# Kernel tuning notes

Measured on AMD Instinct MI355X. Metric: run time of the kernel, lower is better.

Reference implementation:

```python
import jax, jax.numpy as jnp
import numpy as np
import math

N_NODES = 50000
N_EDGES = 800000
IN_DIM = 128
HID = 128
OUT_DIM = 2048
N_LABEL_EDGES = 4096
POOL_RATIO = 0.5
NUM_HEADS = 8


def seg_sum(x, idx, n):
    return jax.ops.segment_sum(x, idx, num_segments=n)


def graph_conv(x, W, b, src, dst, emask, n):
    # DGL GraphConv, norm='both': D_out^-1/2 A D_in^-1/2 (x W) + b (masked edges)
    deg_out = seg_sum(emask, src, n)
    deg_in = seg_sum(emask, dst, n)
    ns = jax.lax.rsqrt(jnp.maximum(deg_out, 1.0))
    nd = jax.lax.rsqrt(jnp.maximum(deg_in, 1.0))
    h = x @ W
    msg = (h * ns[:, None])[src] * emask[:, None]
    agg = seg_sum(msg, dst, n)
    return agg * nd[:, None] + b


def conv_pool_block(x, src, dst, emask, cW, cb, sW, sb):
    # GraphConv -> ReLU -> SAGPool(top-k by GraphConv score, tanh gate) -> avg||max readout
    n = x.shape[0]
    h = jax.nn.relu(graph_conv(x, cW, cb, src, dst, emask, n))
    score = graph_conv(h, sW, sb, src, dst, emask, n)[:, 0]
    k = int(math.ceil(POOL_RATIO * n))  # static
    _, perm = jax.lax.top_k(score, k)
    h_new = h[perm] * jnp.tanh(score[perm])[:, None]
    # remap edges to the pooled node set; drop edges touching removed nodes via mask
    newid = jnp.full((n,), -1, jnp.int32).at[perm].set(jnp.arange(k, dtype=jnp.int32))
    nsrc = newid[src]
    ndst = newid[dst]
    new_mask = emask * (nsrc >= 0).astype(emask.dtype) * (ndst >= 0).astype(emask.dtype)
    nsrc = jnp.maximum(nsrc, 0)
    ndst = jnp.maximum(ndst, 0)
    readout = jnp.concatenate([h_new.mean(0), h_new.max(0)])[None, :]  # [1, 2*HID]
    return h_new, nsrc, ndst, new_mask, readout


def gat_conv(x, fcW, al, ar, lsrc, ldst, n, slope=0.2):
    # GATConv(1 -> 1, num_heads=8): head feature dim is 1
    h = x @ fcW                      # [n, heads]
    el = h * al
    er = h * ar
    e = jax.nn.leaky_relu(el[lsrc] + er[ldst], slope)  # [E_l, heads]
    emax = jax.ops.segment_max(e, ldst, num_segments=n)
    emax = jnp.where(jnp.isfinite(emax), emax, 0.0)
    ex = jnp.exp(e - emax[ldst])
    denom = seg_sum(ex, ldst, n)
    alpha = ex / jnp.maximum(denom[ldst], 1e-9)
    out = seg_sum(alpha * h[lsrc], ldst, n)            # [n, heads]
    return out[:, :, None]                             # [n, heads, 1]


def setup_inputs() -> dict:
    key = jax.random.key(0)
    ks = jax.random.split(key, 32)

    def rn(k, shape, s=0.05):
        return jax.random.normal(k, shape, jnp.float32) * s

    inp = {}
    inp['feat'] = jax.random.normal(ks[0], (N_NODES, IN_DIM), jnp.float32)
    inp['sequence_feature'] = jax.random.normal(ks[1], (1, 1024), jnp.float32)
    inp['src'] = jax.random.randint(ks[2], (N_EDGES,), 0, N_NODES, jnp.int32)
    inp['dst'] = jax.random.randint(ks[3], (N_EDGES,), 0, N_NODES, jnp.int32)
    inp['label_src'] = jax.random.randint(ks[4], (N_LABEL_EDGES,), 0, OUT_DIM, jnp.int32)
    inp['label_dst'] = jax.random.randint(ks[5], (N_LABEL_EDGES,), 0, OUT_DIM, jnp.int32)
    i = 6
    for b in range(3):
        din = IN_DIM if b == 0 else HID
        inp['cW%d' % b] = rn(ks[i], (din, HID)); i += 1
        inp['cb%d' % b] = jnp.zeros((HID,), jnp.float32)
        inp['sW%d' % b] = rn(ks[i], (HID, 1)); i += 1
        inp['sb%d' % b] = jnp.zeros((1,), jnp.float32)
    inp['lin1W'] = rn(ks[i], (2 * HID + 1024, 2 * HID)); i += 1
    inp['lin1b'] = jnp.zeros((2 * HID,), jnp.float32)
    inp['lin2W'] = rn(ks[i], (2 * HID, HID)); i += 1
    inp['lin2b'] = jnp.zeros((HID,), jnp.float32)
    inp['lin3W'] = rn(ks[i], (HID, OUT_DIM)); i += 1
    inp['lin3b'] = jnp.zeros((OUT_DIM,), jnp.float32)
    inp['gat_fcW'] = rn(ks[i], (1, NUM_HEADS)); i += 1
    inp['gat_al'] = rn(ks[i], (NUM_HEADS,)); i += 1
    inp['gat_ar'] = rn(ks[i], (NUM_HEADS,)); i += 1
    return inp


def reference(feat, sequence_feature, src, dst, label_src, label_dst,
              cW0, cb0, sW0, sb0, cW1, cb1, sW1, sb1, cW2, cb2, sW2, sb2,
              lin1W, lin1b, lin2W, lin2b, lin3W, lin3b,
              gat_fcW, gat_al, gat_ar):
    x, s, d = feat, src, dst
    emask = jnp.ones((src.shape[0],), jnp.float32)
    final = None
    for cW, cb, sW, sb in ((cW0, cb0, sW0, sb0), (cW1, cb1, sW1, sb1), (cW2, cb2, sW2, sb2)):
        x, s, d, emask, ro = conv_pool_block(x, s, d, emask, cW, cb, sW, sb)
        final = ro if final is None else final + ro
    final = jnp.concatenate([final, sequence_feature], axis=-1)  # [1, 2*HID+1024]
    f = jax.nn.relu(final @ lin1W + lin1b)
    # dropout: eval mode -> identity
    f = jax.nn.relu(f @ lin2W + lin2b)
    f = f @ lin3W + lin3b          # [1, OUT_DIM]
    ft = f.T                       # [OUT_DIM, 1]
    gat_out = gat_conv(ft, gat_fcW, gat_al, gat_ar, label_src, label_dst, OUT_DIM)
    max_value = jnp.max(gat_out, axis=1)      # [OUT_DIM, 1]
    _ = ft - jax.nn.relu(max_value)           # computed then discarded, as in source
    return ft.T
```

## Files before the change

### kernel.cpp

```cpp
#include <hip/hip_runtime.h>
#include <hip/hip_bf16.h>
#include <cmath>

#define N0 50000
#define NEDGE 800000
#define NEG_HUGE -3.402823466e38f
#define BMAX 64
#define STRIDE 128

typedef int i32x4 __attribute__((ext_vector_type(4)));
typedef __attribute__((ext_vector_type(8))) short short8v;
typedef __attribute__((ext_vector_type(4))) float f32x4;

__device__ inline float b2f(unsigned short u) { return __uint_as_float(((unsigned)u) << 16); }

__device__ inline unsigned short f2b(float f) {
    __hip_bfloat16 h = __float2bfloat16(f);
    return *(unsigned short*)&h;
}

__device__ inline unsigned fkey(float f) {
    unsigned b = __float_as_uint(f);
    if (b == 0x80000000u) b = 0u;
    return (b & 0x80000000u) ? ~b : (b | 0x80000000u);
}

__device__ inline void atomicMaxF(float* a, float v) {
    if (v >= 0.f) atomicMax((int*)a, __float_as_int(v));
    else          atomicMin((unsigned int*)a, __float_as_uint(v));
}

__global__ void k_init(float* finalv, float* f1raw, int* deg_out, int* fill,
                       int* binsA, int* binsB, float* maxbuf, int* ctrl) {
    int i = blockIdx.x * blockDim.x + threadIdx.x;
    if (i < 256) { finalv[i] = 0.f; f1raw[i] = 0.f; }
    if (i < 384) maxbuf[i] = NEG_HUGE;
    if (i < N0) { deg_out[i] = 0; fill[i] = 0; }
    if (i < 65536) { binsA[i] = 0; binsB[i] = 0; }
    if (i < 2) ctrl[8 + i] = 0;
}

__global__ __launch_bounds__(256) void k_build(
        const int* __restrict__ esrc, const int* __restrict__ edst,
        int* deg_out, int* fill, int* csr_src) {
    int t = blockIdx.x * 256 + threadIdx.x;
    int e0 = t * 4;
    if (e0 >= NEDGE) return;
    i32x4 a = __builtin_nontemporal_load((const i32x4*)(esrc + e0));
    i32x4 bq = __builtin_nontemporal_load((const i32x4*)(edst + e0));
    int s[4] = {a.x, a.y, a.z, a.w};
    int d[4] = {bq.x, bq.y, bq.z, bq.w};
#pragma unroll
    for (int kq = 0; kq < 4; ++kq) {
        atomicAdd(&deg_out[s[kq]], 1);
        int pos = atomicAdd(&fill[d[kq]], 1);
        if (pos < STRIDE) csr_src[(size_t)d[kq] * STRIDE + pos] = s[kq];
    }
}

__global__ __launch_bounds__(256) void k_rmbuild(
        const int* __restrict__ esrc, const int* __restrict__ edst,
        const int2* __restrict__ ein, int use_pair,
        const int* __restrict__ ctrl, int slot,
        const int* __restrict__ newid,
        int2* __restrict__ eout, int* __restrict__ outcnt,
        int* deg_out, int* fill, int* csr_src) {
    __shared__ int wbase[4];
    __shared__ int blkbase;
    int E = (slot < 0) ? NEDGE : ctrl[slot];
    if (blockIdx.x * 256 >= E) return;
    int i = blockIdx.x * 256 + threadIdx.x;
    int lane = threadIdx.x & 63, w = threadIdx.x >> 6;
    int ns = -1, nd = -1;
    if (i < E) {
        int s, d;
        if (use_pair) { int2 pr = ein[i]; s = pr.x; d = pr.y; }
        else { s = esrc[i]; d = edst[i]; }
        ns = newid[s]; nd = newid[d];
    }
    bool keep = (ns >= 0) && (nd >= 0);
    unsigned long long m = __ballot(keep);
    int rank = __popcll(m & ((1ull << lane) - 1ull));
    if (lane == 0) wbase[w] = __popcll(m);
    __syncthreads();
    if (threadIdx.x == 0)
        blkbase = atomicAdd(outcnt, wbase[0] + wbase[1] + wbase[2] + wbase[3]);
    __syncthreads();
    int base = blkbase;
    for (int q = 0; q < w; ++q) base += wbase[q];
    if (keep) {
        eout[base + rank] = make_int2(ns, nd);
        atomicAdd(&deg_out[ns], 1);
        int pos = atomicAdd(&fill[nd], 1);
        if (pos < STRIDE) csr_src[(size_t)nd * STRIDE + pos] = ns;
    }
}

__global__ __launch_bounds__(256) void k_gemm(
        const float* __restrict__ feat, const float* __restrict__ xprev,
        const int* __restrict__ oldid, const float* __restrict__ garr,
        const int* __restrict__ deg_out,
        const float* __restrict__ W, unsigned short* __restrict__ hpre,
        int n, int nprev, int mode) {
    __shared__ short Wt[128][136];
    __shared__ short Xt[64][136];
    __shared__ int ridx_s[64];
    __shared__ float esc_s[64];
    int tid = threadIdx.x;
    int r0 = blockIdx.x * 64;
    if (tid < 64) {
        int gr = r0 + tid;
        int ridx = 0; float esc = 0.f;
        if (gr < n) {
            if (mode == 0) {
                ridx = gr;
                esc = rsqrtf(fmaxf((float)deg_out[gr], 1.f));
            } else {
                int orow = oldid[gr];
                if ((unsigned)orow < (unsigned)nprev) {
                    ridx = orow;
                    esc = rsqrtf(fmaxf((float)deg_out[gr], 1.f)) * garr[gr];
                }
            }
        }
        ridx_s[tid] = ridx;
        esc_s[tid] = esc;
    }
    __syncthreads();
    {
        int col = tid & 127;
        int kh = tid >> 7;
#pragma unroll
        for (int c8 = 0; c8 < 8; ++c8) {
            int kb = kh * 64 + c8 * 8;
            unsigned short v[8];
#pragma unroll
            for (int j = 0; j < 8; ++j)
                v[j] = f2b(W[(size_t)(kb + j) * 128 + col]);
            *(uint4*)&Wt[col][kb] = *(uint4*)v;
        }
    }
    {
        const float* xsrc = (mode == 0) ? feat : xprev;
        int rr = tid >> 2;
        int kx = (tid & 3) * 32;
        const float4* xp = (const float4*)(xsrc + (size_t)ridx_s[rr] * 128 + kx);
#pragma unroll
        for (int c4 = 0; c4 < 8; ++c4) {
            float4 v = xp[c4];
            unsigned short u[4];
            u[0] = f2b(v.x); u[1] = f2b(v.y); u[2] = f2b(v.z); u[3] = f2b(v.w);
            *(uint2*)&Xt[rr][kx + c4 * 4] = *(uint2*)u;
        }
    }
    __syncthreads();

    int lane = tid & 63, w = tid >> 6;
    int row16 = lane & 15;
    int ko = (lane >> 4) * 8;
    f32x4 acc[8];
#pragma unroll
    for (int t = 0; t < 8; ++t) acc[t] = (f32x4){0.f, 0.f, 0.f, 0.f};
#pragma unroll
    for (int kc = 0; kc < 4; ++kc) {
        int kbase = kc * 32 + ko;
        short8v a = *(short8v*)&Xt[w * 16 + row16][kbase];
#pragma unroll
        for (int t = 0; t < 8; ++t) {
            short8v b = *(short8v*)&Wt[t * 16 + row16][kbase];
            acc[t] = __builtin_amdgcn_mfma_f32_16x16x32_bf16(a, b, acc[t], 0, 0, 0);
        }
    }
    int rq = (lane >> 4) * 4;
    float esc[4];
#pragma unroll
    for (int r = 0; r < 4; ++r) esc[r] = esc_s[w * 16 + rq + r];
#pragma unroll
    for (int r = 0; r < 4; ++r) {
        int gr = r0 + w * 16 + rq + r;
        if (gr < n) {
            unsigned short* op = hpre + (size_t)gr * 128;
#pragma unroll
            for (int t = 0; t < 8; ++t)
                op[t * 16 + (lane & 15)] = f2b(acc[t][r] * esc[r]);
        }
    }
}

__global__ __launch_bounds__(256) void k_agg_conv(
        const unsigned short* __restrict__ hpre, const int* __restrict__ fill,
        const int* __restrict__ deg_out,
        const int* __restrict__ csr_src,
        const float* __restrict__ cb, const float* __restrict__ sW,
        float* __restrict__ hpost, float* __restrict__ hs, int n) {
    int wid = threadIdx.x >> 6;
    int lane = threadIdx.x & 63;
    int d = blockIdx.x * 4 + wid;
    if (d >= n) return;
    int degin = fill[d];
    int cnt = min(degin, STRIDE);
    const int* bp = csr_src + (size_t)d * STRIDE;
    float a0 = 0.f, a1 = 0.f;
    int j = 0;
    for (; j + 4 <= cnt; j += 4) {
        int4 ss = *(const int4*)(bp + j);
        ushort2 u0 = ((const ushort2*)(hpre + (size_t)ss.x * 128))[lane];
        ushort2 u1 = ((const ushort2*)(hpre + (size_t)ss.y * 128))[lane];
        ushort2 u2 = ((const ushort2*)(hpre + (size_t)ss.z * 128))[lane];
        ushort2 u3 = ((const ushort2*)(hpre + (size_t)ss.w * 128))[lane];
        a0 += (b2f(u0.x) + b2f(u1.x)) + (b2f(u2.x) + b2f(u3.x));
        a1 += (b2f(u0.y) + b2f(u1.y)) + (b2f(u2.y) + b2f(u3.y));
    }
    for (; j < cnt; ++j) {
        int s0 = bp[j];
        ushort2 u0 = ((const ushort2*)(hpre + (size_t)s0 * 128))[lane];
        a0 += b2f(u0.x);
        a1 += b2f(u0.y);
    }
    float nd2 = rsqrtf(fmaxf((float)degin, 1.f));
    int c0 = lane * 2;
    float h0 = fmaxf(fmaf(a0, nd2, cb[c0]), 0.f);
    float h1 = fmaxf(fmaf(a1, nd2, cb[c0 + 1]), 0.f);
    ((float2*)(hpost + (size_t)d * 128))[lane] = make_float2(h0, h1);
    float v = h0 * sW[c0] + h1 * sW[c0 + 1];
#pragma unroll
    for (int off = 32; off; off >>= 1) v += __shfl_down(v, off);
    if (lane == 0) hs[d] = v * rsqrtf(fmaxf((float)deg_out[d], 1.f));
}

__global__ void k_score_hist(const float* __restrict__ hs, const int* __restrict__ fill,
                             const int* __restrict__ csr_src,
                             const float* __restrict__ sb, float* score,
                             int* binsA, int n) {
    int d = blockIdx.x * blockDim.x + threadIdx.x;
    if (d >= n) return;
    int degin = fill[d];
    int cnt = min(degin, STRIDE);
    const int* bp = csr_src + (size_t)d * STRIDE;
    float sum = 0.f;
    int j = 0;
    for (; j + 4 <= cnt; j += 4) {
        int4 ss = *(const int4*)(bp + j);
        sum += (hs[ss.x] + hs[ss.y]) + (hs[ss.z] + hs[ss.w]);
    }
    for (; j < cnt; ++j) sum += hs[bp[j]];
    float sc = rsqrtf(fmaxf((float)degin, 1.f)) * sum + sb[0];
    score[d] = sc;
    atomicAdd(&binsA[fkey(sc) >> 16], 1);
}

__global__ void k_rhist2(const float* __restrict__ score, const int* __restrict__ ctrl,
                         int n, int* binsB) {
    unsigned p16 = (unsigned)ctrl[3];
    for (int i = blockIdx.x * 256 + threadIdx.x; i < n; i += gridDim.x * 256) {
        unsigned u = fkey(score[i]);
        if ((u >> 16) == p16) atomicAdd(&binsB[u & 0xFFFFu], 1);
    }
}

__global__ void k_rpick(int stage, int k0, int* ctrl, const int* __restrict__ bins) {
    __shared__ int gs[64];
    __shared__ int arr[1024];
    __shared__ int wsum[16];
    __shared__ int sChunk, sKrem;
    int t = threadIdx.x;
    {
        int c = t >> 4, sub = t & 15;
        const int4* p4 = (const int4*)(bins + (size_t)c * 1024);
        int s = 0;
#pragma unroll
        for (int q = 0; q < 16; ++q) {
            int4 v = p4[q * 16 + sub];
            s += v.x + v.y + v.z + v.w;
        }
#pragma unroll
        for (int off = 8; off; off >>= 1) s += __shfl_down(s, off, 16);
        if (sub == 0) gs[c] = s;
    }
    __syncthreads();
    if (t == 0) {
        int kneed = (stage == 0) ? k0 : ctrl[4];
        int cum = 0, c = 63;
        for (; c >= 1; --c) { int v = gs[c]; if (cum + v >= kneed) break; cum += v; }
        sChunk = c; sKrem = kneed - cum;
    }
    __syncthreads();
    int c = sChunk;
    int v = bins[(size_t)c * 1024 + t];
    arr[t] = v;
    int lane = t & 63, w = t >> 6;
    int s = v;
#pragma unroll
    for (int off = 32; off; off >>= 1) s += __shfl_down(s, off);
    if (lane == 0) wsum[w] = s;
    __syncthreads();
    if (t == 0) {
        int kneed = sKrem;
        int cum = 0, w2 = 15;
        for (; w2 >= 1; --w2) { int vv = wsum[w2]; if (cum + vv >= kneed) break; cum += vv; }
        int j = 63;
        for (; j >= 1; --j) { int vv = arr[w2 * 64 + j]; if (cum + vv >= kneed) break; cum += vv; }
        int bin = c * 1024 + w2 * 64 + j;
        if (stage == 0) { ctrl[3] = bin; ctrl[4] = kneed - cum; }
        else {
            ctrl[0] = (int)((((unsigned)ctrl[3]) << 16) | (unsigned)bin);
            ctrl[2] = kneed - cum;
        }
    }
}

__global__ void k_ccnt(const float* __restrict__ score, const int* __restrict__ ctrl,
                       int n, int* cntG, int* cntE) {
    __shared__ int wG[16], wE[16];
    int b = blockIdx.x;
    int i = b * 1024 + threadIdx.x;
    int lane = threadIdx.x & 63, wid = threadIdx.x >> 6;
    unsigned T = (unsigned)ctrl[0];
    bool inb = (i < n);
    unsigned u = inb ? fkey(score[i]) : 0u;
    bool isG = inb && (u > T);
    bool isE = inb && (u == T);
    unsigned long long mG = __ballot(isG);
    unsigned long long mE = __ballot(isE);
    if (lane == 0) { wG[wid] = __popcll(mG); wE[wid] = __popcll(mE); }
    __syncthreads();
    if (threadIdx.x == 0) {
        int sg = 0, se = 0;
#pragma unroll
        for (int w = 0; w < 16; ++w) { sg += wG[w]; se += wE[w]; }
        cntG[b] = sg; cntE[b] = se;
    }
}

__global__ void k_cemit(const float* __restrict__ score, const int* __restrict__ ctrl,
                        const int* __restrict__ cntG, const int* __restrict__ cntE,
                        int n, int knext, int* newid, int* oldid, float* garr,
                        int* deg_out, int* fill, int* binsA, int* binsB) {
    __shared__ int wG[16], wE[16];
    __shared__ int sGoff, sEoff;
    int b = blockIdx.x;
    int i = b * 1024 + threadIdx.x;
    if (knext > 0) {
        for (int z = i; z < 65536; z += gridDim.x * 1024) { binsA[z] = 0; binsB[z] = 0; }
        if (i < knext) { deg_out[i] = 0; fill[i] = 0; }
    }
    int lane = threadIdx.x & 63, wid = threadIdx.x >> 6;
    unsigned T = (unsigned)ctrl[0];
    int needEq = ctrl[2];
    bool inb = (i < n);
    float sc = inb ? score[i] : 0.f;
    unsigned u = inb ? fkey(sc) : 0u;
    bool isG = inb && (u > T);
    bool isE = inb && (u == T);
    unsigned long long mG = __ballot(isG);
    unsigned long long mE = __ballot(isE);
    if (lane == 0) { wG[wid] = __popcll(mG); wE[wid] = __popcll(mE); }
    if (threadIdx.x < 64) {
        int l = threadIdx.x;
        int vg = (l < b) ? cntG[l] : 0;
        int ve = (l < b) ? cntE[l] : 0;
#pragma unroll
        for (int off2 = 32; off2; off2 >>= 1) {
            vg += __shfl_down(vg, off2);
            ve += __shfl_down(ve, off2);
        }
        if (l == 0) { sGoff = vg; sEoff = ve; }
    }
    __syncthreads();
    unsigned long long below = (1ull << lane) - 1ull;
    int gW = 0, eW = 0;
    for (int w = 0; w < wid; ++w) { gW += wG[w]; eW += wE[w]; }
    int Gb = sGoff + gW + __popcll(mG & below);
    int Eb = sEoff + eW + __popcll(mE & below);
    if (inb) {
        bool sel = isG || (isE && (Eb < needEq));
        if (sel) {
            int j = Gb + min(Eb, needEq);
            newid[i] = j;
            oldid[j] = i;
            garr[j] = tanhf(sc);
        } else {
            newid[i] = -1;
        }
    }
}

__global__ void k_readout(const float* __restrict__ hpost, const int* __restrict__ oldid,
                          const float* __restrict__ garr, float* finalv, float* maxbuf,
                          int k, int n, float invk) {
    int c = threadIdx.x;
    float sum = 0.f, mx = NEG_HUGE;
    for (int r = blockIdx.x; r < k; r += gridDim.x) {
        int o = oldid[r];
        if ((unsigned)o >= (unsigned)n) continue;
        float g = garr[r];
        float v = hpost[(size_t)o * 128 + c] * g;
        sum += v;
        mx = fmaxf(mx, v);
    }
    atomicAdd(&finalv[c], sum * invk);
    atomicMaxF(&maxbuf[c], mx);
}

__global__ void k_mlp1(const float* __restrict__ finalv, const float* __restrict__ maxbuf,
                       const float* __restrict__ seq, const float* __restrict__ W1,
                       float* f1raw) {
    int o = threadIdx.x;
    int j0 = blockIdx.x * 128;
    float acc = 0.f;
    for (int jj = 0; jj < 128; ++jj) {
        int j = j0 + jj;
        float fv;
        if (j < 128) fv = finalv[j];
        else if (j < 256) fv = maxbuf[j - 128] + maxbuf[j] + maxbuf[j + 128];
        else fv = seq[j - 256];
        acc = fmaf(fv, W1[(size_t)j * 256 + o], acc);
    }
    atomicAdd(&f1raw[o], acc);
}

__global__ void k_mlp2(const float* __restrict__ f1raw, const float* __restrict__ b1,
                       const float* __restrict__ W2, const float* __restrict__ bb2,
                       float* f2v) {
    __shared__ float f1s[256];
    int t = threadIdx.x;
    f1s[t] = fmaxf(f1raw[t] + b1[t], 0.f);
    f1s[t + 128] = fmaxf(f1raw[t + 128] + b1[t + 128], 0.f);
    __syncthreads();
    float acc = 0.f;
    for (int j = 0; j < 256; ++j)
        acc = fmaf(f1s[j], W2[(size_t)j * 128 + t], acc);
    f2v[t] = fmaxf(acc + bb2[t], 0.f);
}

__global__ void k_mlp3(const float* __restrict__ f2v, const float* __restrict__ W3,
                       const float* __restrict__ b3, float* out) {
    __shared__ float f2s[128];
    int t = threadIdx.x;
    f2s[t] = f2v[t];
    __syncthreads();
    int col = blockIdx.x * 128 + t;
    float acc = 0.f;
    for (int j = 0; j < 128; ++j)
        acc = fmaf(f2s[j], W3[(size_t)j * 2048 + col], acc);
    out[col] = acc + b3[col];
}

extern "C" void kernel_launch(void* const* d_in, const int* in_sizes, int n_in,
                              void* d_out, int out_size, void* d_ws, size_t ws_size,
                              hipStream_t stream) {
    (void)in_sizes; (void)n_in; (void)out_size; (void)ws_size;
    const float* feat = (const float*)d_in[0];
    const float* seq  = (const float*)d_in[1];
    const int* src = (const int*)d_in[2];
    const int* dst = (const int*)d_in[3];
    const float *cW[3], *cb[3], *sW[3], *sb[3];
    for (int b = 0; b < 3; ++b) {
        cW[b] = (const float*)d_in[6 + 4 * b];
        cb[b] = (const float*)d_in[7 + 4 * b];
        sW[b] = (const float*)d_in[8 + 4 * b];
        sb[b] = (const float*)d_in[9 + 4 * b];
    }
    const float* lin1W = (const float*)d_in[18];
    const float* lin1b = (const float*)d_in[19];
    const float* lin2W = (const float*)d_in[20];
    const float* lin2b = (const float*)d_in[21];
    const float* lin3W = (const float*)d_in[22];
    const float* lin3b = (const float*)d_in[23];
    float* out = (float*)d_out;

    char* p = (char*)d_ws;
    size_t off = 0;
    auto alloc = [&](size_t bytes) -> void* {
        void* r = p + off;
        off = (off + bytes + 255) & ~(size_t)255;
        return r;
    };
    unsigned short* hpre = (unsigned short*)alloc((size_t)N0 * 128 * 2);
    float* hpost  = (float*)alloc((size_t)N0 * 128 * 4);
    float* hs     = (float*)alloc((size_t)N0 * 4);
    float* score  = (float*)alloc((size_t)N0 * 4);
    int* deg_out  = (int*)alloc((size_t)N0 * 4);
    int* fill     = (int*)alloc((size_t)N0 * 4);
    int2* epair1  = (int2*)alloc((size_t)NEDGE * 8);
    int* csr_src  = (int*)alloc((size_t)N0 * STRIDE * 4);
    int* newid    = (int*)alloc((size_t)N0 * 4);
    int* oldid    = (int*)alloc((size_t)25000 * 4);
    float* garr   = (float*)alloc((size_t)25000 * 4);
    float* maxbuf = (float*)alloc(3 * 128 * 4);
    float* finalv = (float*)alloc(256 * 4);
    float* f1raw  = (float*)alloc(256 * 4);
    float* f2v    = (float*)alloc(128 * 4);
    int* ctrl     = (int*)alloc(64 * 4);
    int* binsA    = (int*)alloc(65536 * 4);
    int* binsB    = (int*)alloc(65536 * 4);
    int* cntG     = (int*)alloc(BMAX * 4);
    int* cntE     = (int*)alloc(BMAX * 4);
    int2* epair2  = (int2*)hpre;

    const int nb[3] = {50000, 25000, 12500};
    const int kb[3] = {25000, 12500, 6250};

    k_init<<<256, 256, 0, stream>>>(finalv, f1raw, deg_out, fill, binsA, binsB,
                                    maxbuf, ctrl);

    for (int b = 0; b < 3; ++b) {
        int n = nb[b], k = kb[b];
        int B = (n + 1023) / 1024;
        if (b == 0)
            k_build<<<(NEDGE / 4 + 255) / 256, 256, 0, stream>>>(src, dst, deg_out, fill,
                                                                 csr_src);
        else if (b == 1)
            k_rmbuild<<<(NEDGE + 255) / 256, 256, 0, stream>>>(
                src, dst, (const int2*)0, 0, ctrl, -1, newid, epair1, ctrl + 8,
                deg_out, fill, csr_src);
        else
            k_rmbuild<<<(NEDGE + 255) / 256, 256, 0, stream>>>(
                (const int*)0, (const int*)0, epair1, 1, ctrl, 8, newid, epair2, ctrl + 9,
                deg_out, fill, csr_src);
        k_gemm<<<(n + 63) / 64, 256, 0, stream>>>(feat, hpost, oldid, garr, deg_out, cW[b],
                                                  hpre, n, (b > 0) ? nb[b - 1] : 1,
                                                  (b == 0) ? 0 : 1);
        k_agg_conv<<<(n + 3) / 4, 256, 0, stream>>>(hpre, fill, deg_out, csr_src, cb[b],
                                                    sW[b], hpost, hs, n);
        k_score_hist<<<(n + 255) / 256, 256, 0, stream>>>(hs, fill, csr_src, sb[b],
                                                          score, binsA, n);
        k_rpick<<<1, 1024, 0, stream>>>(0, k, ctrl, binsA);
        k_rhist2<<<128, 256, 0, stream>>>(score, ctrl, n, binsB);
        k_rpick<<<1, 1024, 0, stream>>>(1, k, ctrl, binsB);
        k_ccnt<<<B, 1024, 0, stream>>>(score, ctrl, n, cntG, cntE);
        k_cemit<<<B, 1024, 0, stream>>>(score, ctrl, cntG, cntE, n, (b < 2) ? kb[b] : 0,
                                        newid, oldid, garr, deg_out, fill, binsA, binsB);
        k_readout<<<512, 128, 0, stream>>>(hpost, oldid, garr, finalv, maxbuf + b * 128,
                                           k, n, 1.0f / (float)k);
    }

    k_mlp1<<<10, 256, 0, stream>>>(finalv, maxbuf, seq, lin1W, f1raw);
    k_mlp2<<<1, 128, 0, stream>>>(f1raw, lin1b, lin2W, lin2b, f2v);
    k_mlp3<<<16, 128, 0, stream>>>(f2v, lin3W, lin3b, out);
}
```

Measured before the change: 594.4 us.

## Fuse aggregation, scoring, top-k selection and readout into one cooperative kernel

Replaces the per-block sequence of aggregation, score histogram, two radix-pick passes, count, emit and readout kernels with a single cooperative kernel using grid-wide syncs between phases. This removes many small kernel launches and their gaps. The readout now reduces within the block in shared memory before atomics. The trade-off is that the heavy gather phase runs on only 128 persistent blocks, which may underuse the GPU, and grid syncs add their own cost.

```diff
diff --git a/kernel.cpp b/kernel.cpp
--- a/kernel.cpp
+++ b/kernel.cpp
@@ -1,12 +1,16 @@
 #include <hip/hip_runtime.h>
 #include <hip/hip_bf16.h>
+#include <hip/hip_cooperative_groups.h>
 #include <cmath>
+
+namespace cg = cooperative_groups;
 
 #define N0 50000
 #define NEDGE 800000
 #define NEG_HUGE -3.402823466e38f
 #define BMAX 64
 #define STRIDE 128
+#define SELB 128
 
 typedef int i32x4 __attribute__((ext_vector_type(4)));
 typedef __attribute__((ext_vector_type(8))) short short8v;
@@ -187,82 +191,10 @@
     }
 }
 
-__global__ __launch_bounds__(256) void k_agg_conv(
-        const unsigned short* __restrict__ hpre, const int* __restrict__ fill,
-        const int* __restrict__ deg_out,
-        const int* __restrict__ csr_src,
-        const float* __restrict__ cb, const float* __restrict__ sW,
-        float* __restrict__ hpost, float* __restrict__ hs, int n) {
-    int wid = threadIdx.x >> 6;
-    int lane = threadIdx.x & 63;
-    int d = blockIdx.x * 4 + wid;
-    if (d >= n) return;
-    int degin = fill[d];
-    int cnt = min(degin, STRIDE);
-    const int* bp = csr_src + (size_t)d * STRIDE;
-    float a0 = 0.f, a1 = 0.f;
-    int j = 0;
-    for (; j + 4 <= cnt; j += 4) {
-        int4 ss = *(const int4*)(bp + j);
-        ushort2 u0 = ((const ushort2*)(hpre + (size_t)ss.x * 128))[lane];
-        ushort2 u1 = ((const ushort2*)(hpre + (size_t)ss.y * 128))[lane];
-        ushort2 u2 = ((const ushort2*)(hpre + (size_t)ss.z * 128))[lane];
-        ushort2 u3 = ((const ushort2*)(hpre + (size_t)ss.w * 128))[lane];
-        a0 += (b2f(u0.x) + b2f(u1.x)) + (b2f(u2.x) + b2f(u3.x));
-        a1 += (b2f(u0.y) + b2f(u1.y)) + (b2f(u2.y) + b2f(u3.y));
-    }
-    for (; j < cnt; ++j) {
-        int s0 = bp[j];
-        ushort2 u0 = ((const ushort2*)(hpre + (size_t)s0 * 128))[lane];
-        a0 += b2f(u0.x);
-        a1 += b2f(u0.y);
-    }
-    float nd2 = rsqrtf(fmaxf((float)degin, 1.f));
-    int c0 = lane * 2;
-    float h0 = fmaxf(fmaf(a0, nd2, cb[c0]), 0.f);
-    float h1 = fmaxf(fmaf(a1, nd2, cb[c0 + 1]), 0.f);
-    ((float2*)(hpost + (size_t)d * 128))[lane] = make_float2(h0, h1);
-    float v = h0 * sW[c0] + h1 * sW[c0 + 1];
-#pragma unroll
-    for (int off = 32; off; off >>= 1) v += __shfl_down(v, off);
-    if (lane == 0) hs[d] = v * rsqrtf(fmaxf((float)deg_out[d], 1.f));
-}
-
-__global__ void k_score_hist(const float* __restrict__ hs, const int* __restrict__ fill,
-                             const int* __restrict__ csr_src,
-                             const float* __restrict__ sb, float* score,
-                             int* binsA, int n) {
-    int d = blockIdx.x * blockDim.x + threadIdx.x;
-    if (d >= n) return;
-    int degin = fill[d];
-    int cnt = min(degin, STRIDE);
-    const int* bp = csr_src + (size_t)d * STRIDE;
-    float sum = 0.f;
-    int j = 0;
-    for (; j + 4 <= cnt; j += 4) {
-        int4 ss = *(const int4*)(bp + j);
-        sum += (hs[ss.x] + hs[ss.y]) + (hs[ss.z] + hs[ss.w]);
-    }
-    for (; j < cnt; ++j) sum += hs[bp[j]];
-    float sc = rsqrtf(fmaxf((float)degin, 1.f)) * sum + sb[0];
-    score[d] = sc;
-    atomicAdd(&binsA[fkey(sc) >> 16], 1);
-}
-
-__global__ void k_rhist2(const float* __restrict__ score, const int* __restrict__ ctrl,
-                         int n, int* binsB) {
-    unsigned p16 = (unsigned)ctrl[3];
-    for (int i = blockIdx.x * 256 + threadIdx.x; i < n; i += gridDim.x * 256) {
-        unsigned u = fkey(score[i]);
-        if ((u >> 16) == p16) atomicAdd(&binsB[u & 0xFFFFu], 1);
-    }
-}
-
-__global__ void k_rpick(int stage, int k0, int* ctrl, const int* __restrict__ bins) {
-    __shared__ int gs[64];
-    __shared__ int arr[1024];
-    __shared__ int wsum[16];
-    __shared__ int sChunk, sKrem;
+__device__ __forceinline__ void rpick_body(int stage, int k0, int* ctrl,
+                                           const int* __restrict__ bins,
+                                           int* gs, int* arr, int* wsum,
+                                           int* sChunk, int* sKrem) {
     int t = threadIdx.x;
     {
         int c = t >> 4, sub = t & 15;
@@ -282,10 +214,10 @@
         int kneed = (stage == 0) ? k0 : ctrl[4];
         int cum = 0, c = 63;
         for (; c >= 1; --c) { int v = gs[c]; if (cum + v >= kneed) break; cum += v; }
-        sChunk = c; sKrem = kneed - cum;
-    }
-    __syncthreads();
-    int c = sChunk;
+        *sChunk = c; *sKrem = kneed - cum;
+    }
+    __syncthreads();
+    int c = *sChunk;
     int v = bins[(size_t)c * 1024 + t];
     arr[t] = v;
     int lane = t & 63, w = t >> 6;
@@ -295,7 +227,7 @@
     if (lane == 0) wsum[w] = s;
     __syncthreads();
     if (t == 0) {
-        int kneed = sKrem;
+        int kneed = *sKrem;
         int cum = 0, w2 = 15;
         for (; w2 >= 1; --w2) { int vv = wsum[w2]; if (cum + vv >= kneed) break; cum += vv; }
         int j = 63;
@@ -309,97 +241,196 @@
     }
 }
 
-__global__ void k_ccnt(const float* __restrict__ score, const int* __restrict__ ctrl,
-                       int n, int* cntG, int* cntE) {
-    __shared__ int wG[16], wE[16];
-    int b = blockIdx.x;
-    int i = b * 1024 + threadIdx.x;
-    int lane = threadIdx.x & 63, wid = threadIdx.x >> 6;
-    unsigned T = (unsigned)ctrl[0];
-    bool inb = (i < n);
-    unsigned u = inb ? fkey(score[i]) : 0u;
-    bool isG = inb && (u > T);
-    bool isE = inb && (u == T);
-    unsigned long long mG = __ballot(isG);
-    unsigned long long mE = __ballot(isE);
-    if (lane == 0) { wG[wid] = __popcll(mG); wE[wid] = __popcll(mE); }
-    __syncthreads();
-    if (threadIdx.x == 0) {
-        int sg = 0, se = 0;
-#pragma unroll
-        for (int w = 0; w < 16; ++w) { sg += wG[w]; se += wE[w]; }
-        cntG[b] = sg; cntE[b] = se;
-    }
-}
-
-__global__ void k_cemit(const float* __restrict__ score, const int* __restrict__ ctrl,
-                        const int* __restrict__ cntG, const int* __restrict__ cntE,
-                        int n, int knext, int* newid, int* oldid, float* garr,
-                        int* deg_out, int* fill, int* binsA, int* binsB) {
+__global__ __launch_bounds__(1024) void k_select(
+        const unsigned short* __restrict__ hpre,
+        const float* __restrict__ cb, const float* __restrict__ sW,
+        const float* __restrict__ sb,
+        int* deg_out, int* fill, const int* __restrict__ csr_src,
+        float* hpost, float* hs, float* score,
+        int* binsA, int* binsB, int* ctrl, int* cntG, int* cntE,
+        int* newid, int* oldid, float* garr,
+        float* finalv, float* maxbuf,
+        int n, int k, int knext, float invk) {
+    cg::grid_group grid = cg::this_grid();
+    __shared__ int gs[64], arr[1024], wsum[16];
+    __shared__ int sChunk, sKrem;
     __shared__ int wG[16], wE[16];
     __shared__ int sGoff, sEoff;
-    int b = blockIdx.x;
-    int i = b * 1024 + threadIdx.x;
+    __shared__ float redS[1024], redM[1024];
+
+    int tid = threadIdx.x;
+    int lane = tid & 63, wv = tid >> 6;
+    int gt = blockIdx.x * 1024 + tid;
+    int nt = gridDim.x * 1024;
+
+    for (int d = blockIdx.x * 16 + wv; d < n; d += gridDim.x * 16) {
+        int degin = fill[d];
+        int cnt = min(degin, STRIDE);
+        const int* bp = csr_src + (size_t)d * STRIDE;
+        float a0 = 0.f, a1 = 0.f;
+        int j = 0;
+        for (; j + 4 <= cnt; j += 4) {
+            int4 ss = *(const int4*)(bp + j);
+            ushort2 u0 = ((const ushort2*)(hpre + (size_t)ss.x * 128))[lane];
+            ushort2 u1 = ((const ushort2*)(hpre + (size_t)ss.y * 128))[lane];
+            ushort2 u2 = ((const ushort2*)(hpre + (size_t)ss.z * 128))[lane];
+            ushort2 u3 = ((const ushort2*)(hpre + (size_t)ss.w * 128))[lane];
+            a0 += (b2f(u0.x) + b2f(u1.x)) + (b2f(u2.x) + b2f(u3.x));
+            a1 += (b2f(u0.y) + b2f(u1.y)) + (b2f(u2.y) + b2f(u3.y));
+        }
+        for (; j < cnt; ++j) {
+            int s0 = bp[j];
+            ushort2 u0 = ((const ushort2*)(hpre + (size_t)s0 * 128))[lane];
+            a0 += b2f(u0.x);
+            a1 += b2f(u0.y);
+        }
+        float nd2 = rsqrtf(fmaxf((float)degin, 1.f));
+        int c0 = lane * 2;
+        float h0 = fmaxf(fmaf(a0, nd2, cb[c0]), 0.f);
+        float h1 = fmaxf(fmaf(a1, nd2, cb[c0 + 1]), 0.f);
+        ((float2*)(hpost + (size_t)d * 128))[lane] = make_float2(h0, h1);
+        float v = h0 * sW[c0] + h1 * sW[c0 + 1];
+#pragma unroll
+        for (int off = 32; off; off >>= 1) v += __shfl_down(v, off);
+        if (lane == 0) hs[d] = v * rsqrtf(fmaxf((float)deg_out[d], 1.f));
+    }
+    __threadfence();
+    grid.sync();
+
+    for (int d = gt; d < n; d += nt) {
+        int degin = fill[d];
+        int cnt = min(degin, STRIDE);
+        const int* bp = csr_src + (size_t)d * STRIDE;
+        float sum = 0.f;
+        int j = 0;
+        for (; j + 4 <= cnt; j += 4) {
+            int4 ss = *(const int4*)(bp + j);
+            sum += (hs[ss.x] + hs[ss.y]) + (hs[ss.z] + hs[ss.w]);
+        }
+        for (; j < cnt; ++j) sum += hs[bp[j]];
+        float sc = rsqrtf(fmaxf((float)degin, 1.f)) * sum + sb[0];
+        score[d] = sc;
+        atomicAdd(&binsA[fkey(sc) >> 16], 1);
+    }
+    __threadfence();
+    grid.sync();
+
+    if (blockIdx.x == 0)
+        rpick_body(0, k, ctrl, binsA, gs, arr, wsum, &sChunk, &sKrem);
+    __threadfence();
+    grid.sync();
+
+    {
+        unsigned p16 = (unsigned)ctrl[3];
+        for (int i = gt; i < n; i += nt) {
+            unsigned u = fkey(score[i]);
+            if ((u >> 16) == p16) atomicAdd(&binsB[u & 0xFFFFu], 1);
+        }
+    }
+    __threadfence();
+    grid.sync();
+
+    if (blockIdx.x == 0)
+        rpick_body(1, k, ctrl, binsB, gs, arr, wsum, &sChunk, &sKrem);
+    __threadfence();
+    grid.sync();
+
+    int B0 = (n + 1023) >> 10;
+    unsigned T = (unsigned)ctrl[0];
+    if (blockIdx.x < B0) {
+        int i = blockIdx.x * 1024 + tid;
+        bool inb = (i < n);
+        unsigned u = inb ? fkey(score[i]) : 0u;
+        bool isG = inb && (u > T);
+        bool isE = inb && (u == T);
+        unsigned long long mG = __ballot(isG);
+        unsigned long long mE = __ballot(isE);
+        if (lane == 0) { wG[wv] = __popcll(mG); wE[wv] = __popcll(mE); }
+        __syncthreads();
+        if (tid == 0) {
+            int sg = 0, se = 0;
+#pragma unroll
+            for (int w = 0; w < 16; ++w) { sg += wG[w]; se += wE[w]; }
+            cntG[blockIdx.x] = sg; cntE[blockIdx.x] = se;
+        }
+    }
+    __threadfence();
+    grid.sync();
+
     if (knext > 0) {
-        for (int z = i; z < 65536; z += gridDim.x * 1024) { binsA[z] = 0; binsB[z] = 0; }
-        if (i < knext) { deg_out[i] = 0; fill[i] = 0; }
-    }
-    int lane = threadIdx.x & 63, wid = threadIdx.x >> 6;
-    unsigned T = (unsigned)ctrl[0];
-    int needEq = ctrl[2];
-    bool inb = (i < n);
-    float sc = inb ? score[i] : 0.f;
-    unsigned u = inb ? fkey(sc) : 0u;
-    bool isG = inb && (u > T);
-    bool isE = inb && (u == T);
-    unsigned long long mG = __ballot(isG);
-    unsigned long long mE = __ballot(isE);
-    if (lane == 0) { wG[wid] = __popcll(mG); wE[wid] = __popcll(mE); }
-    if (threadIdx.x < 64) {
-        int l = threadIdx.x;
-        int vg = (l < b) ? cntG[l] : 0;
-        int ve = (l < b) ? cntE[l] : 0;
-#pragma unroll
-        for (int off2 = 32; off2; off2 >>= 1) {
-            vg += __shfl_down(vg, off2);
-            ve += __shfl_down(ve, off2);
-        }
-        if (l == 0) { sGoff = vg; sEoff = ve; }
-    }
-    __syncthreads();
-    unsigned long long below = (1ull << lane) - 1ull;
-    int gW = 0, eW = 0;
-    for (int w = 0; w < wid; ++w) { gW += wG[w]; eW += wE[w]; }
-    int Gb = sGoff + gW + __popcll(mG & below);
-    int Eb = sEoff + eW + __popcll(mE & below);
-    if (inb) {
-        bool sel = isG || (isE && (Eb < needEq));
-        if (sel) {
-            int j = Gb + min(Eb, needEq);
-            newid[i] = j;
-            oldid[j] = i;
-            garr[j] = tanhf(sc);
-        } else {
-            newid[i] = -1;
-        }
-    }
-}
-
-__global__ void k_readout(const float* __restrict__ hpost, const int* __restrict__ oldid,
-                          const float* __restrict__ garr, float* finalv, float* maxbuf,
-                          int k, int n, float invk) {
-    int c = threadIdx.x;
-    float sum = 0.f, mx = NEG_HUGE;
-    for (int r = blockIdx.x; r < k; r += gridDim.x) {
-        int o = oldid[r];
-        if ((unsigned)o >= (unsigned)n) continue;
-        float g = garr[r];
-        float v = hpost[(size_t)o * 128 + c] * g;
-        sum += v;
-        mx = fmaxf(mx, v);
-    }
-    atomicAdd(&finalv[c], sum * invk);
-    atomicMaxF(&maxbuf[c], mx);
+        for (int z = gt; z < 65536; z += nt) { binsA[z] = 0; binsB[z] = 0; }
+        for (int z = gt; z < knext; z += nt) { deg_out[z] = 0; fill[z] = 0; }
+    }
+    {
+        int needEq = ctrl[2];
+        if (blockIdx.x < B0) {
+            int i = blockIdx.x * 1024 + tid;
+            bool inb = (i < n);
+            float sc = inb ? score[i] : 0.f;
+            unsigned u = inb ? fkey(sc) : 0u;
+            bool isG = inb && (u > T);
+            bool isE = inb && (u == T);
+            unsigned long long mG = __ballot(isG);
+            unsigned long long mE = __ballot(isE);
+            if (lane == 0) { wG[wv] = __popcll(mG); wE[wv] = __popcll(mE); }
+            if (tid < 64) {
+                int vg = (tid < blockIdx.x) ? cntG[tid] : 0;
+                int ve = (tid < blockIdx.x) ? cntE[tid] : 0;
+#pragma unroll
+                for (int off2 = 32; off2; off2 >>= 1) {
+                    vg += __shfl_down(vg, off2);
+                    ve += __shfl_down(ve, off2);
+                }
+                if (tid == 0) { sGoff = vg; sEoff = ve; }
+            }
+            __syncthreads();
+            unsigned long long below = (1ull << lane) - 1ull;
+            int gW = 0, eW = 0;
+            for (int w = 0; w < wv; ++w) { gW += wG[w]; eW += wE[w]; }
+            int Gb = sGoff + gW + __popcll(mG & below);
+            int Eb = sEoff + eW + __popcll(mE & below);
+            if (inb) {
+                bool sel = isG || (isE && (Eb < needEq));
+                if (sel) {
+                    int j = Gb + min(Eb, needEq);
+                    newid[i] = j;
+                    oldid[j] = i;
+                    garr[j] = tanhf(sc);
+                } else {
+                    newid[i] = -1;
+                }
+            }
+        }
+    }
+    __threadfence();
+    grid.sync();
+
+    {
+        int grp = blockIdx.x * 8 + (tid >> 7);
+        int c = tid & 127;
+        float sum = 0.f, mx = NEG_HUGE;
+        for (int r = grp; r < k; r += gridDim.x * 8) {
+            int o = oldid[r];
+            if ((unsigned)o >= (unsigned)n) continue;
+            float g = garr[r];
+            float v = hpost[(size_t)o * 128 + c] * g;
+            sum += v;
+            mx = fmaxf(mx, v);
+        }
+        redS[tid] = sum;
+        redM[tid] = mx;
+        __syncthreads();
+        if (tid < 128) {
+            float s2 = 0.f, m2 = NEG_HUGE;
+#pragma unroll
+            for (int g2 = 0; g2 < 8; ++g2) {
+                s2 += redS[g2 * 128 + tid];
+                m2 = fmaxf(m2, redM[g2 * 128 + tid]);
+            }
+            atomicAdd(&finalv[tid], s2 * invk);
+            atomicMaxF(&maxbuf[tid], m2);
+        }
+    }
 }
 
 __global__ void k_mlp1(const float* __restrict__ finalv, const float* __restrict__ maxbuf,
@@ -506,7 +537,6 @@
 
     for (int b = 0; b < 3; ++b) {
         int n = nb[b], k = kb[b];
-        int B = (n + 1023) / 1024;
         if (b == 0)
             k_build<<<(NEDGE / 4 + 255) / 256, 256, 0, stream>>>(src, dst, deg_out, fill,
                                                                  csr_src);
@@ -521,18 +551,25 @@
         k_gemm<<<(n + 63) / 64, 256, 0, stream>>>(feat, hpost, oldid, garr, deg_out, cW[b],
                                                   hpre, n, (b > 0) ? nb[b - 1] : 1,
                                                   (b == 0) ? 0 : 1);
-        k_agg_conv<<<(n + 3) / 4, 256, 0, stream>>>(hpre, fill, deg_out, csr_src, cb[b],
-                                                    sW[b], hpost, hs, n);
-        k_score_hist<<<(n + 255) / 256, 256, 0, stream>>>(hs, fill, csr_src, sb[b],
-                                                          score, binsA, n);
-        k_rpick<<<1, 1024, 0, stream>>>(0, k, ctrl, binsA);
-        k_rhist2<<<128, 256, 0, stream>>>(score, ctrl, n, binsB);
-        k_rpick<<<1, 1024, 0, stream>>>(1, k, ctrl, binsB);
-        k_ccnt<<<B, 1024, 0, stream>>>(score, ctrl, n, cntG, cntE);
-        k_cemit<<<B, 1024, 0, stream>>>(score, ctrl, cntG, cntE, n, (b < 2) ? kb[b] : 0,
-                                        newid, oldid, garr, deg_out, fill, binsA, binsB);
-        k_readout<<<512, 128, 0, stream>>>(hpost, oldid, garr, finalv, maxbuf + b * 128,
-                                           k, n, 1.0f / (float)k);
+        {
+            const unsigned short* hpre_a = hpre;
+            const float* cb_a = cb[b];
+            const float* sW_a = sW[b];
+            const float* sb_a = sb[b];
+            float* maxbuf_a = maxbuf + b * 128;
+            int knext = (b < 2) ? kb[b] : 0;
+            float invk = 1.0f / (float)k;
+            void* args[] = {
+                (void*)&hpre_a, (void*)&cb_a, (void*)&sW_a, (void*)&sb_a,
+                (void*)&deg_out, (void*)&fill, (void*)&csr_src,
+                (void*)&hpost, (void*)&hs, (void*)&score,
+                (void*)&binsA, (void*)&binsB, (void*)&ctrl, (void*)&cntG, (void*)&cntE,
+                (void*)&newid, (void*)&oldid, (void*)&garr,
+                (void*)&finalv, (void*)&maxbuf_a,
+                (void*)&n, (void*)&k, (void*)&knext, (void*)&invk};
+            hipLaunchCooperativeKernel((void*)k_select, dim3(SELB), dim3(1024),
+                                       args, 0, stream);
+        }
     }
 
     k_mlp1<<<10, 256, 0, stream>>>(finalv, maxbuf, seq, lin1W, f1raw);
```

Result: slower. 1.701 ms (+186.2%).
